# Performance work log

Measured on AMD Instinct MI355X. Metric: run time of the kernel, lower is better.

The kernel has to match this reference:

```python
import jax, jax.numpy as jnp
import numpy as np

EPS = 1e-5

def setup_inputs() -> dict:
    key = jax.random.key(0)
    ks = jax.random.split(key, 8)
    B, s, i, c = 1, 256, 256, 256
    h, d = 8, 32  # n_head, c_h; h*d == c
    m = jax.random.normal(ks[0], (B, s, i, c), dtype=jnp.float32)
    msa_mask = jnp.ones((B, s, i), dtype=jnp.float32)
    sc = 1.0 / np.sqrt(c)
    return {
        "m": m,
        "msa_mask": msa_mask,
        "ln_w": jnp.ones((c,), jnp.float32),
        "ln_b": jnp.zeros((c,), jnp.float32),
        "wq": jax.random.normal(ks[1], (h * d, c), jnp.float32) * sc,
        "wk": jax.random.normal(ks[2], (h * d, c), jnp.float32) * sc,
        "wv": jax.random.normal(ks[3], (h * d, c), jnp.float32) * sc,
        "wg": jax.random.normal(ks[4], (h * d, c), jnp.float32) * sc,
        "bg": jnp.zeros((h * d,), jnp.float32),
        "wo": jax.random.normal(ks[5], (c, h * d), jnp.float32) * sc,
        "bo": jnp.zeros((c,), jnp.float32),
    }

def _to_heads(x, B, s, i, h, d):
    # [B,s,i,h*d] -> [B,i,h,s,d]
    return jnp.transpose(x.reshape(B, s, i, h, d), (0, 2, 3, 1, 4))

def reference(m, msa_mask, ln_w, ln_b, wq, wk, wv, wg, bg, wo, bo):
    B, s, i, c = m.shape
    hd = wq.shape[0]
    d = 32
    h = hd // d
    # LayerNorm over channel dim
    mu = jnp.mean(m, axis=-1, keepdims=True)
    var = jnp.mean(jnp.square(m - mu), axis=-1, keepdims=True)
    m_norm = (m - mu) * jax.lax.rsqrt(var + EPS) * ln_w + ln_b
    q = _to_heads(m_norm @ wq.T, B, s, i, h, d)
    k = _to_heads(m_norm @ wk.T, B, s, i, h, d)
    v = _to_heads(m_norm @ wv.T, B, s, i, h, d)
    gate = jax.nn.sigmoid(_to_heads(m_norm @ wg.T + bg, B, s, i, h, d))
    # masks: msa_mask [B,s,i] -> keys mask [B,i,s]
    mk = jnp.transpose(msa_mask, (0, 2, 1)) > 0
    mv = mk.astype(q.dtype)[:, :, None, :, None]  # [B,i,1,s,1]
    q = q * mv
    k = k * mv
    v = v * mv
    gate = gate * mv
    # attention over sequence dim s (per column i)
    logits = jnp.einsum('bihqd,bihkd->bihqk', q, k) / jnp.sqrt(jnp.asarray(d, q.dtype))
    pair_mask = (mk[:, :, None, :] & mk[:, :, :, None])[:, :, None, :, :]  # [B,i,1,s,s]
    logits = jnp.where(pair_mask, logits, jnp.asarray(-1e9, q.dtype))
    attn = jax.nn.softmax(logits, axis=-1)
    o = jnp.einsum('bihqk,bihkd->bihqd', attn, v)
    o = o * gate * mv
    # [B,i,h,s,d] -> [B,i,s,h*d]
    o = jnp.transpose(o, (0, 1, 3, 2, 4)).reshape(B, i, s, h * d)
    o = o @ wo.T + bo  # [B,i,s,c]
    return jnp.transpose(o, (0, 2, 1, 3))  # [B,s,i,c]
```

## Files before the change

### kernel.cpp

```cpp
#include <hip/hip_runtime.h>

typedef unsigned short u16;
typedef unsigned int u32;
typedef __attribute__((ext_vector_type(8))) short short8;
typedef __attribute__((ext_vector_type(4))) float f32x4;

constexpr int S_ = 256, I_ = 256, C_ = 256, H_ = 8, D_ = 32, HD_ = 256;
constexpr float QSCALE = 0.17677669529663687f;

__device__ __forceinline__ float b2f(u32 u) {
  union { u32 i; float f; } x; x.i = u << 16; return x.f;
}
__device__ __forceinline__ u16 f2b(float f) {
  union { float f; u32 i; } x; x.f = f;
  u32 r = x.i + 0x7fffu + ((x.i >> 16) & 1u);
  return (u16)(r >> 16);
}
__device__ __forceinline__ uint4 pack8(const float* f) {
  uint4 r;
  r.x = (u32)f2b(f[0]) | ((u32)f2b(f[1]) << 16);
  r.y = (u32)f2b(f[2]) | ((u32)f2b(f[3]) << 16);
  r.z = (u32)f2b(f[4]) | ((u32)f2b(f[5]) << 16);
  r.w = (u32)f2b(f[6]) | ((u32)f2b(f[7]) << 16);
  return r;
}
__device__ __forceinline__ void load8f(const float* p, float* f) {
  float4 a = *reinterpret_cast<const float4*>(p);
  float4 b = *reinterpret_cast<const float4*>(p + 4);
  f[0] = a.x; f[1] = a.y; f[2] = a.z; f[3] = a.w;
  f[4] = b.x; f[5] = b.y; f[6] = b.z; f[7] = b.w;
}
__device__ __forceinline__ f32x4 mfma16(short8 a, short8 b, f32x4 c) {
  return __builtin_amdgcn_mfma_f32_16x16x32_bf16(a, b, c, 0, 0, 0);
}

__global__ void k_lnnorm(const float* __restrict__ m, const float* __restrict__ mask,
                         const float* __restrict__ lnw, const float* __restrict__ lnb,
                         u16* __restrict__ mn) {
  int wg = (blockIdx.x * 256 + threadIdx.x) >> 6;
  int lane = threadIdx.x & 63;
  float4 wv = *reinterpret_cast<const float4*>(lnw + lane * 4);
  float4 bv = *reinterpret_cast<const float4*>(lnb + lane * 4);
  for (int it = 0; it < 8; ++it) {
    int row = wg * 8 + it;
    float4 v = *reinterpret_cast<const float4*>(m + (size_t)row * C_ + lane * 4);
    float s = v.x + v.y + v.z + v.w;
    float ss = v.x * v.x + v.y * v.y + v.z * v.z + v.w * v.w;
#pragma unroll
    for (int o = 32; o; o >>= 1) { s += __shfl_xor(s, o); ss += __shfl_xor(ss, o); }
    float mean = s * (1.f / C_);
    float var = ss * (1.f / C_) - mean * mean;
    float rs = rsqrtf(fmaxf(var, 0.f) + 1e-5f);
    float mk = mask[row];
    float y[4];
    y[0] = ((v.x - mean) * rs * wv.x + bv.x) * mk;
    y[1] = ((v.y - mean) * rs * wv.y + bv.y) * mk;
    y[2] = ((v.z - mean) * rs * wv.z + bv.z) * mk;
    y[3] = ((v.w - mean) * rs * wv.w + bv.w) * mk;
    uint2 pk;
    pk.x = (u32)f2b(y[0]) | ((u32)f2b(y[1]) << 16);
    pk.y = (u32)f2b(y[2]) | ((u32)f2b(y[3]) << 16);
    *reinterpret_cast<uint2*>(mn + (size_t)row * C_ + lane * 4) = pk;
  }
}

__global__ void k_wpack(const float* __restrict__ wq, const float* __restrict__ wk,
                        const float* __restrict__ wv, const float* __restrict__ wg,
                        const float* __restrict__ wo, u16* __restrict__ wall2) {
  int gid = blockIdx.x * 4 + (threadIdx.x >> 6);
  int lane = threadIdx.x & 63;
  if (gid >= 640) return;
  const float* W;
  int g2;
  if (gid < 512) {
    int mat = gid >> 7;
    W = (mat == 0) ? wq : (mat == 1) ? wk : (mat == 2) ? wv : wg;
    g2 = gid & 127;
  } else {
    W = wo;
    g2 = gid - 512;
  }
  int nn = g2 & 1, kk = (g2 >> 1) & 7, ch2 = (g2 >> 4) & 1, cbi = (g2 >> 5) & 3;
  int row = cbi * 64 + ch2 * 32 + nn * 16 + (lane & 15);
  int k0 = kk * 32 + (lane >> 4) * 8;
  float f[8];
  load8f(W + (size_t)row * 256 + k0, f);
  *reinterpret_cast<uint4*>(wall2 + (size_t)gid * 512 + lane * 8) = pack8(f);
}

__global__ __launch_bounds__(256, 4) void k_qkvg(
    const u16* __restrict__ mn, const float* __restrict__ mask,
    const u16* __restrict__ wall2, const float* __restrict__ bg,
    u16* __restrict__ qws, u16* __restrict__ kws, u16* __restrict__ vws,
    u16* __restrict__ gws) {
  __shared__ u16 lA[64 * 256];
  int tile = blockIdx.x;
  int i_col = tile >> 2, s0 = (tile & 3) * 64;
  int t = threadIdx.x;
  int rowg = t >> 5, cg = t & 31;
#pragma unroll
  for (int p = 0; p < 8; ++p) {
    int row = p * 8 + rowg;
    int rg = (s0 + row) * I_ + i_col;
    *reinterpret_cast<uint4*>(&lA[row * 256 + ((cg * 8) ^ ((row & 7) << 3))]) =
        *reinterpret_cast<const uint4*>(mn + (size_t)rg * C_ + cg * 8);
  }
  __syncthreads();
  int lane = t & 63, w = t >> 6;
  int wr = (w >> 1) * 32, ch2 = w & 1, wc = ch2 * 32;
  int lr = lane & 15, lk = lane >> 4;
  f32x4 zz = {0.f, 0.f, 0.f, 0.f};
  for (int chunk = 0; chunk < 16; ++chunk) {
    int mat = chunk >> 2, cb = (chunk & 3) * 64;
    const u16* Bp = wall2 + (size_t)((chunk * 2 + ch2) * 16) * 512 + lane * 8;
    f32x4 acc[2][2] = {{zz, zz}, {zz, zz}};
#pragma unroll
    for (int kk = 0; kk < 8; ++kk) {
      int kb = kk * 32 + lk * 8;
      int ra0 = wr + lr, ra1 = wr + 16 + lr;
      short8 a0 = *reinterpret_cast<const short8*>(&lA[ra0 * 256 + (kb ^ ((ra0 & 7) << 3))]);
      short8 a1 = *reinterpret_cast<const short8*>(&lA[ra1 * 256 + (kb ^ ((ra1 & 7) << 3))]);
      short8 b0 = *reinterpret_cast<const short8*>(Bp + (kk * 2 + 0) * 512);
      short8 b1 = *reinterpret_cast<const short8*>(Bp + (kk * 2 + 1) * 512);
      acc[0][0] = mfma16(a0, b0, acc[0][0]);
      acc[0][1] = mfma16(a0, b1, acc[0][1]);
      acc[1][0] = mfma16(a1, b0, acc[1][0]);
      acc[1][1] = mfma16(a1, b1, acc[1][1]);
    }
#pragma unroll
    for (int mm = 0; mm < 2; ++mm) {
#pragma unroll
      for (int nn = 0; nn < 2; ++nn) {
        int colL = wc + nn * 16 + lr;
        int hd = cb + colL;
        int h = hd >> 5, d = hd & 31;
        if (mat == 2) {
          int sbase = s0 + wr + mm * 16 + lk * 4;
          uint2 pk;
          pk.x = (u32)f2b(acc[mm][nn][0]) | ((u32)f2b(acc[mm][nn][1]) << 16);
          pk.y = (u32)f2b(acc[mm][nn][2]) | ((u32)f2b(acc[mm][nn][3]) << 16);
          *reinterpret_cast<uint2*>(
              vws + (((size_t)i_col * H_ + h) * D_ + d) * S_ + sbase) = pk;
        } else {
          u16* dstp = (mat == 0) ? qws : (mat == 1) ? kws : gws;
          float bgv = (mat == 3) ? bg[hd] : 0.f;
#pragma unroll
          for (int r = 0; r < 4; ++r) {
            int rowL = wr + mm * 16 + lk * 4 + r;
            int s = s0 + rowL;
            float v = acc[mm][nn][r];
            if (mat == 0) v *= QSCALE;
            if (mat == 3) {
              float mkv = mask[s * I_ + i_col];
              v = mkv * (1.f / (1.f + __expf(-(v + bgv))));
            }
            dstp[(((size_t)i_col * H_ + h) * S_ + s) * D_ + d] = f2b(v);
          }
        }
      }
    }
  }
}

__global__ __launch_bounds__(1024) void k_attn(
    u16* __restrict__ qws, const u16* __restrict__ kws,
    const u16* __restrict__ vws, const u16* __restrict__ gws,
    const float* __restrict__ mask) {
  __shared__ u16 lK[256 * 40];
  __shared__ u16 lV[32 * 264];
  __shared__ float lMk[256];
  int bid = blockIdx.x;
  int i = bid >> 3, h = bid & 7;
  int t = threadIdx.x;
  size_t base = ((size_t)i * H_ + h) * (size_t)(S_ * D_);
  {
    int s = t >> 2, part = t & 3;
    *reinterpret_cast<uint4*>(&lK[s * 40 + part * 8]) =
        *reinterpret_cast<const uint4*>(kws + base + s * 32 + part * 8);
    int d = t >> 5, p2 = t & 31;
    *reinterpret_cast<uint4*>(&lV[d * 264 + p2 * 8]) =
        *reinterpret_cast<const uint4*>(vws + base + d * 256 + p2 * 8);
    if (t < 256) lMk[t] = mask[t * I_ + i];
  }
  __syncthreads();
  int lane = t & 63;
  int wvid = t >> 6;
  int lq = lane & 15, g = lane >> 4;
  int qbase = wvid * 16;
  short8 qf = *reinterpret_cast<const short8*>(qws + base + (size_t)(qbase + lq) * D_ + g * 8);
  f32x4 zz = {0.f, 0.f, 0.f, 0.f};
  f32x4 o0 = zz, o1 = zz;
  float mcur = -1e30f, sumd = 0.f;
  int addrP0 = (lq + ((g & 1) * 2 + 0) * 16) * 4;
  int addrP1 = (lq + ((g & 1) * 2 + 1) * 16) * 4;
  int aC0 = (g * 4 + 0) * 4, aC1 = (g * 4 + 1) * 4;
  int aC2 = (g * 4 + 2) * 4, aC3 = (g * 4 + 3) * 4;
#pragma unroll
  for (int ks = 0; ks < 8; ++ks) {
    int k0 = ks * 32;
    short8 kf0 = *reinterpret_cast<const short8*>(&lK[(k0 + lq) * 40 + g * 8]);
    short8 kf1 = *reinterpret_cast<const short8*>(&lK[(k0 + 16 + lq) * 40 + g * 8]);
    f32x4 s0 = mfma16(kf0, qf, zz);
    f32x4 s1 = mfma16(kf1, qf, zz);
    float4 mk0 = *reinterpret_cast<const float4*>(&lMk[k0 + g * 4]);
    float4 mk1 = *reinterpret_cast<const float4*>(&lMk[k0 + 16 + g * 4]);
    float sv[8];
    sv[0] = mk0.x > 0.f ? s0[0] : -1e9f;
    sv[1] = mk0.y > 0.f ? s0[1] : -1e9f;
    sv[2] = mk0.z > 0.f ? s0[2] : -1e9f;
    sv[3] = mk0.w > 0.f ? s0[3] : -1e9f;
    sv[4] = mk1.x > 0.f ? s1[0] : -1e9f;
    sv[5] = mk1.y > 0.f ? s1[1] : -1e9f;
    sv[6] = mk1.z > 0.f ? s1[2] : -1e9f;
    sv[7] = mk1.w > 0.f ? s1[3] : -1e9f;
    float tmax = fmaxf(fmaxf(fmaxf(sv[0], sv[1]), fmaxf(sv[2], sv[3])),
                       fmaxf(fmaxf(sv[4], sv[5]), fmaxf(sv[6], sv[7])));
    tmax = fmaxf(tmax, __shfl_xor(tmax, 16));
    tmax = fmaxf(tmax, __shfl_xor(tmax, 32));
    float mnew = fmaxf(mcur, tmax);
    float c = __expf(mcur - mnew);
    mcur = mnew;
    float p[8];
#pragma unroll
    for (int j = 0; j < 8; ++j) p[j] = __expf(sv[j] - mnew);
    sumd = sumd * c + ((p[0] + p[1]) + (p[2] + p[3])) + ((p[4] + p[5]) + (p[6] + p[7]));
    u32 pk00 = (u32)f2b(p[0]) | ((u32)f2b(p[1]) << 16);
    u32 pk01 = (u32)f2b(p[2]) | ((u32)f2b(p[3]) << 16);
    u32 pk10 = (u32)f2b(p[4]) | ((u32)f2b(p[5]) << 16);
    u32 pk11 = (u32)f2b(p[6]) | ((u32)f2b(p[7]) << 16);
    int b00 = __builtin_amdgcn_ds_bpermute(addrP0, (int)pk00);
    int b10 = __builtin_amdgcn_ds_bpermute(addrP0, (int)pk10);
    int b01 = __builtin_amdgcn_ds_bpermute(addrP0, (int)pk01);
    int b11 = __builtin_amdgcn_ds_bpermute(addrP0, (int)pk11);
    int b02 = __builtin_amdgcn_ds_bpermute(addrP1, (int)pk00);
    int b12 = __builtin_amdgcn_ds_bpermute(addrP1, (int)pk10);
    int b03 = __builtin_amdgcn_ds_bpermute(addrP1, (int)pk01);
    int b13 = __builtin_amdgcn_ds_bpermute(addrP1, (int)pk11);
    union { int u[4]; short8 s8; } pu;
    bool lo = (g < 2);
    pu.u[0] = lo ? b00 : b10;
    pu.u[1] = lo ? b01 : b11;
    pu.u[2] = lo ? b02 : b12;
    pu.u[3] = lo ? b03 : b13;
    float co0 = __int_as_float(__builtin_amdgcn_ds_bpermute(aC0, __float_as_int(c)));
    float co1 = __int_as_float(__builtin_amdgcn_ds_bpermute(aC1, __float_as_int(c)));
    float co2 = __int_as_float(__builtin_amdgcn_ds_bpermute(aC2, __float_as_int(c)));
    float co3 = __int_as_float(__builtin_amdgcn_ds_bpermute(aC3, __float_as_int(c)));
    o0[0] *= co0; o0[1] *= co1; o0[2] *= co2; o0[3] *= co3;
    o1[0] *= co0; o1[1] *= co1; o1[2] *= co2; o1[3] *= co3;
    short8 vf0 = *reinterpret_cast<const short8*>(&lV[lq * 264 + k0 + g * 8]);
    short8 vf1 = *reinterpret_cast<const short8*>(&lV[(16 + lq) * 264 + k0 + g * 8]);
    o0 = mfma16(pu.s8, vf0, o0);
    o1 = mfma16(pu.s8, vf1, o1);
  }
  float s2 = sumd + __shfl_xor(sumd, 16);
  float tot = s2 + __shfl_xor(s2, 32);
  float iv = 1.f / tot;
  float ivo[4];
  ivo[0] = __int_as_float(__builtin_amdgcn_ds_bpermute(aC0, __float_as_int(iv)));
  ivo[1] = __int_as_float(__builtin_amdgcn_ds_bpermute(aC1, __float_as_int(iv)));
  ivo[2] = __int_as_float(__builtin_amdgcn_ds_bpermute(aC2, __float_as_int(iv)));
  ivo[3] = __int_as_float(__builtin_amdgcn_ds_bpermute(aC3, __float_as_int(iv)));
#pragma unroll
  for (int r = 0; r < 4; ++r) {
    int row = qbase + g * 4 + r;
    size_t idx0 = base + (size_t)row * D_ + lq;
    size_t idx1 = idx0 + 16;
    float g0 = b2f((u32)gws[idx0]);
    float g1 = b2f((u32)gws[idx1]);
    qws[idx0] = f2b(o0[r] * ivo[r] * g0);
    qws[idx1] = f2b(o1[r] * ivo[r] * g1);
  }
}

__global__ __launch_bounds__(256, 4) void k_oproj(const u16* __restrict__ ows,
                                                  const u16* __restrict__ wall2,
                                                  const float* __restrict__ bo,
                                                  float* __restrict__ out) {
  __shared__ u16 lA[64 * 256];
  int tile = blockIdx.x;
  int r0 = tile * 64;
  int t = threadIdx.x;
  int rowg = t >> 5, cg = t & 31;
  int hh = cg >> 2, d0 = (cg & 3) * 8;
#pragma unroll
  for (int p = 0; p < 8; ++p) {
    int row = p * 8 + rowg;
    int rg = r0 + row;
    int ii = rg >> 8, ss = rg & 255;
    *reinterpret_cast<uint4*>(&lA[row * 256 + ((cg * 8) ^ ((row & 7) << 3))]) =
        *reinterpret_cast<const uint4*>(ows + (((size_t)ii * H_ + hh) * S_ + ss) * D_ + d0);
  }
  __syncthreads();
  int lane = t & 63, w = t >> 6;
  int wr = (w >> 1) * 32, ch2 = w & 1, wc = ch2 * 32;
  int lr = lane & 15, lk = lane >> 4;
  f32x4 zz = {0.f, 0.f, 0.f, 0.f};
  for (int chunk = 0; chunk < 4; ++chunk) {
    int cb = chunk * 64;
    const u16* Bp = wall2 + (size_t)(512 + (chunk * 2 + ch2) * 16) * 512 + lane * 8;
    f32x4 acc[2][2] = {{zz, zz}, {zz, zz}};
#pragma unroll
    for (int kk = 0; kk < 8; ++kk) {
      int kb = kk * 32 + lk * 8;
      int ra0 = wr + lr, ra1 = wr + 16 + lr;
      short8 a0 = *reinterpret_cast<const short8*>(&lA[ra0 * 256 + (kb ^ ((ra0 & 7) << 3))]);
      short8 a1 = *reinterpret_cast<const short8*>(&lA[ra1 * 256 + (kb ^ ((ra1 & 7) << 3))]);
      short8 b0 = *reinterpret_cast<const short8*>(Bp + (kk * 2 + 0) * 512);
      short8 b1 = *reinterpret_cast<const short8*>(Bp + (kk * 2 + 1) * 512);
      acc[0][0] = mfma16(a0, b0, acc[0][0]);
      acc[0][1] = mfma16(a0, b1, acc[0][1]);
      acc[1][0] = mfma16(a1, b0, acc[1][0]);
      acc[1][1] = mfma16(a1, b1, acc[1][1]);
    }
#pragma unroll
    for (int mm = 0; mm < 2; ++mm) {
#pragma unroll
      for (int nn = 0; nn < 2; ++nn) {
        int colL = wc + nn * 16 + lr;
        int ch = cb + colL;
        float bov = bo[ch];
#pragma unroll
        for (int r = 0; r < 4; ++r) {
          int rowL = wr + mm * 16 + lk * 4 + r;
          int rg = r0 + rowL;
          int ii = rg >> 8;
          int ss = rg & 255;
          out[((size_t)ss * I_ + ii) * C_ + ch] = acc[mm][nn][r] + bov;
        }
      }
    }
  }
}

extern "C" void kernel_launch(void* const* d_in, const int* in_sizes, int n_in,
                              void* d_out, int out_size, void* d_ws, size_t ws_size,
                              hipStream_t stream) {
  const float *m, *mask, *lnw, *lnb, *wq, *wk, *wv, *wg, *bg, *wo, *bo;
  if (in_sizes[0] > 1000000) {
    m = (const float*)d_in[0]; mask = (const float*)d_in[1];
    lnw = (const float*)d_in[2]; lnb = (const float*)d_in[3];
    wq = (const float*)d_in[4]; wk = (const float*)d_in[5];
    wv = (const float*)d_in[6]; wg = (const float*)d_in[7];
    bg = (const float*)d_in[8]; wo = (const float*)d_in[9];
    bo = (const float*)d_in[10];
  } else {
    bg = (const float*)d_in[0]; bo = (const float*)d_in[1];
    lnb = (const float*)d_in[2]; lnw = (const float*)d_in[3];
    m = (const float*)d_in[4]; mask = (const float*)d_in[5];
    wg = (const float*)d_in[6]; wk = (const float*)d_in[7];
    wo = (const float*)d_in[8]; wq = (const float*)d_in[9];
    wv = (const float*)d_in[10];
  }
  float* out = (float*)d_out;

  const size_t SZ = (size_t)S_ * I_ * C_;
  u16* qws = (u16*)d_ws;
  u16* kws = qws + SZ;
  u16* vws = kws + SZ;
  u16* gws = vws + SZ;
  u16* mn = gws + SZ;
  u16* wall2 = mn + SZ;

  k_lnnorm<<<2048, 256, 0, stream>>>(m, mask, lnw, lnb, mn);
  k_wpack<<<160, 256, 0, stream>>>(wq, wk, wv, wg, wo, wall2);
  k_qkvg<<<1024, 256, 0, stream>>>(mn, mask, wall2, bg, qws, kws, vws, gws);
  k_attn<<<2048, 1024, 0, stream>>>(qws, kws, vws, gws, mask);
  k_oproj<<<1024, 256, 0, stream>>>(qws, wall2, bo, out);
}
```

Baseline: 193.2 us.

## Fuse LayerNorm into QKVG projection and double threads per GEMM block

Removes the separate LayerNorm kernel and its bf16 intermediate buffer by computing mean/variance and normalisation inside the QKVG GEMM's LDS load stage, reading fp32 input directly. Both the QKVG and output-projection kernels now run 512 threads per block, with warps split across output chunks so each warp handles half as many chunks. This cuts one launch and a full write plus read of the normalised activations. In exchange each QKVG block reads twice the bytes from fp32 input, and the larger blocks may lower the number of blocks resident per CU.

```diff
diff --git a/kernel.cpp b/kernel.cpp
--- a/kernel.cpp
+++ b/kernel.cpp
@@ -32,36 +32,6 @@
 }
 __device__ __forceinline__ f32x4 mfma16(short8 a, short8 b, f32x4 c) {
   return __builtin_amdgcn_mfma_f32_16x16x32_bf16(a, b, c, 0, 0, 0);
-}
-
-__global__ void k_lnnorm(const float* __restrict__ m, const float* __restrict__ mask,
-                         const float* __restrict__ lnw, const float* __restrict__ lnb,
-                         u16* __restrict__ mn) {
-  int wg = (blockIdx.x * 256 + threadIdx.x) >> 6;
-  int lane = threadIdx.x & 63;
-  float4 wv = *reinterpret_cast<const float4*>(lnw + lane * 4);
-  float4 bv = *reinterpret_cast<const float4*>(lnb + lane * 4);
-  for (int it = 0; it < 8; ++it) {
-    int row = wg * 8 + it;
-    float4 v = *reinterpret_cast<const float4*>(m + (size_t)row * C_ + lane * 4);
-    float s = v.x + v.y + v.z + v.w;
-    float ss = v.x * v.x + v.y * v.y + v.z * v.z + v.w * v.w;
-#pragma unroll
-    for (int o = 32; o; o >>= 1) { s += __shfl_xor(s, o); ss += __shfl_xor(ss, o); }
-    float mean = s * (1.f / C_);
-    float var = ss * (1.f / C_) - mean * mean;
-    float rs = rsqrtf(fmaxf(var, 0.f) + 1e-5f);
-    float mk = mask[row];
-    float y[4];
-    y[0] = ((v.x - mean) * rs * wv.x + bv.x) * mk;
-    y[1] = ((v.y - mean) * rs * wv.y + bv.y) * mk;
-    y[2] = ((v.z - mean) * rs * wv.z + bv.z) * mk;
-    y[3] = ((v.w - mean) * rs * wv.w + bv.w) * mk;
-    uint2 pk;
-    pk.x = (u32)f2b(y[0]) | ((u32)f2b(y[1]) << 16);
-    pk.y = (u32)f2b(y[2]) | ((u32)f2b(y[3]) << 16);
-    *reinterpret_cast<uint2*>(mn + (size_t)row * C_ + lane * 4) = pk;
-  }
 }
 
 __global__ void k_wpack(const float* __restrict__ wq, const float* __restrict__ wk,
@@ -88,8 +58,9 @@
   *reinterpret_cast<uint4*>(wall2 + (size_t)gid * 512 + lane * 8) = pack8(f);
 }
 
-__global__ __launch_bounds__(256, 4) void k_qkvg(
-    const u16* __restrict__ mn, const float* __restrict__ mask,
+__global__ __launch_bounds__(512) void k_qkvg(
+    const float* __restrict__ m, const float* __restrict__ mask,
+    const float* __restrict__ lnw, const float* __restrict__ lnb,
     const u16* __restrict__ wall2, const float* __restrict__ bg,
     u16* __restrict__ qws, u16* __restrict__ kws, u16* __restrict__ vws,
     u16* __restrict__ gws) {
@@ -98,20 +69,41 @@
   int i_col = tile >> 2, s0 = (tile & 3) * 64;
   int t = threadIdx.x;
   int rowg = t >> 5, cg = t & 31;
-#pragma unroll
-  for (int p = 0; p < 8; ++p) {
-    int row = p * 8 + rowg;
+  float wv8[8], bv8[8];
+  load8f(lnw + cg * 8, wv8);
+  load8f(lnb + cg * 8, bv8);
+#pragma unroll
+  for (int p = 0; p < 4; ++p) {
+    int row = p * 16 + rowg;
     int rg = (s0 + row) * I_ + i_col;
-    *reinterpret_cast<uint4*>(&lA[row * 256 + ((cg * 8) ^ ((row & 7) << 3))]) =
-        *reinterpret_cast<const uint4*>(mn + (size_t)rg * C_ + cg * 8);
+    float xf[8], yf[8];
+    load8f(m + (size_t)rg * C_ + cg * 8, xf);
+    float s1 = 0.f, s2 = 0.f;
+#pragma unroll
+    for (int u = 0; u < 8; ++u) { s1 += xf[u]; s2 += xf[u] * xf[u]; }
+#pragma unroll
+    for (int o = 16; o; o >>= 1) { s1 += __shfl_xor(s1, o); s2 += __shfl_xor(s2, o); }
+    float mean = s1 * (1.f / C_);
+    float var = s2 * (1.f / C_) - mean * mean;
+    float rs = rsqrtf(fmaxf(var, 0.f) + 1e-5f);
+    float mkv = mask[rg];
+#pragma unroll
+    for (int u = 0; u < 8; ++u) yf[u] = ((xf[u] - mean) * rs * wv8[u] + bv8[u]) * mkv;
+    *reinterpret_cast<uint4*>(&lA[row * 256 + ((cg * 8) ^ ((row & 7) << 3))]) = pack8(yf);
   }
   __syncthreads();
   int lane = t & 63, w = t >> 6;
-  int wr = (w >> 1) * 32, ch2 = w & 1, wc = ch2 * 32;
+  int wr = (w >> 2) * 32;
+  int dsel = (w & 3) >> 1;
+  int ch2 = w & 1;
+  int wc = ch2 * 32;
   int lr = lane & 15, lk = lane >> 4;
   f32x4 zz = {0.f, 0.f, 0.f, 0.f};
-  for (int chunk = 0; chunk < 16; ++chunk) {
-    int mat = chunk >> 2, cb = (chunk & 3) * 64;
+#pragma unroll
+  for (int it = 0; it < 8; ++it) {
+    int chunk = it * 2 + dsel;
+    const int mat = it >> 1;
+    int cb = (chunk & 3) * 64;
     const u16* Bp = wall2 + (size_t)((chunk * 2 + ch2) * 16) * 512 + lane * 8;
     f32x4 acc[2][2] = {{zz, zz}, {zz, zz}};
 #pragma unroll
@@ -127,6 +119,7 @@
       acc[1][0] = mfma16(a1, b0, acc[1][0]);
       acc[1][1] = mfma16(a1, b1, acc[1][1]);
     }
+    u16* dstp = (mat == 0) ? qws : (mat == 1) ? kws : (mat == 2) ? vws : gws;
 #pragma unroll
     for (int mm = 0; mm < 2; ++mm) {
 #pragma unroll
@@ -139,15 +132,12 @@
           uint2 pk;
           pk.x = (u32)f2b(acc[mm][nn][0]) | ((u32)f2b(acc[mm][nn][1]) << 16);
           pk.y = (u32)f2b(acc[mm][nn][2]) | ((u32)f2b(acc[mm][nn][3]) << 16);
-          *reinterpret_cast<uint2*>(
-              vws + (((size_t)i_col * H_ + h) * D_ + d) * S_ + sbase) = pk;
+          *reinterpret_cast<uint2*>(vws + (((size_t)i_col * H_ + h) * D_ + d) * S_ + sbase) = pk;
         } else {
-          u16* dstp = (mat == 0) ? qws : (mat == 1) ? kws : gws;
           float bgv = (mat == 3) ? bg[hd] : 0.f;
 #pragma unroll
           for (int r = 0; r < 4; ++r) {
-            int rowL = wr + mm * 16 + lk * 4 + r;
-            int s = s0 + rowL;
+            int s = s0 + wr + mm * 16 + lk * 4 + r;
             float v = acc[mm][nn][r];
             if (mat == 0) v *= QSCALE;
             if (mat == 3) {
@@ -273,10 +263,10 @@
   }
 }
 
-__global__ __launch_bounds__(256, 4) void k_oproj(const u16* __restrict__ ows,
-                                                  const u16* __restrict__ wall2,
-                                                  const float* __restrict__ bo,
-                                                  float* __restrict__ out) {
+__global__ __launch_bounds__(512) void k_oproj(const u16* __restrict__ ows,
+                                               const u16* __restrict__ wall2,
+                                               const float* __restrict__ bo,
+                                               float* __restrict__ out) {
   __shared__ u16 lA[64 * 256];
   int tile = blockIdx.x;
   int r0 = tile * 64;
@@ -284,8 +274,8 @@
   int rowg = t >> 5, cg = t & 31;
   int hh = cg >> 2, d0 = (cg & 3) * 8;
 #pragma unroll
-  for (int p = 0; p < 8; ++p) {
-    int row = p * 8 + rowg;
+  for (int p = 0; p < 4; ++p) {
+    int row = p * 16 + rowg;
     int rg = r0 + row;
     int ii = rg >> 8, ss = rg & 255;
     *reinterpret_cast<uint4*>(&lA[row * 256 + ((cg * 8) ^ ((row & 7) << 3))]) =
@@ -293,10 +283,15 @@
   }
   __syncthreads();
   int lane = t & 63, w = t >> 6;
-  int wr = (w >> 1) * 32, ch2 = w & 1, wc = ch2 * 32;
+  int wr = (w >> 2) * 32;
+  int dsel = (w & 3) >> 1;
+  int ch2 = w & 1;
+  int wc = ch2 * 32;
   int lr = lane & 15, lk = lane >> 4;
   f32x4 zz = {0.f, 0.f, 0.f, 0.f};
-  for (int chunk = 0; chunk < 4; ++chunk) {
+#pragma unroll
+  for (int it = 0; it < 2; ++it) {
+    int chunk = it * 2 + dsel;
     int cb = chunk * 64;
     const u16* Bp = wall2 + (size_t)(512 + (chunk * 2 + ch2) * 16) * 512 + lane * 8;
     f32x4 acc[2][2] = {{zz, zz}, {zz, zz}};
@@ -317,13 +312,11 @@
     for (int mm = 0; mm < 2; ++mm) {
 #pragma unroll
       for (int nn = 0; nn < 2; ++nn) {
-        int colL = wc + nn * 16 + lr;
-        int ch = cb + colL;
+        int ch = cb + wc + nn * 16 + lr;
         float bov = bo[ch];
 #pragma unroll
         for (int r = 0; r < 4; ++r) {
-          int rowL = wr + mm * 16 + lk * 4 + r;
-          int rg = r0 + rowL;
+          int rg = r0 + wr + mm * 16 + lk * 4 + r;
           int ii = rg >> 8;
           int ss = rg & 255;
           out[((size_t)ss * I_ + ii) * C_ + ch] = acc[mm][nn][r] + bov;
@@ -359,12 +352,10 @@
   u16* kws = qws + SZ;
   u16* vws = kws + SZ;
   u16* gws = vws + SZ;
-  u16* mn = gws + SZ;
-  u16* wall2 = mn + SZ;
-
-  k_lnnorm<<<2048, 256, 0, stream>>>(m, mask, lnw, lnb, mn);
+  u16* wall2 = gws + SZ;
+
   k_wpack<<<160, 256, 0, stream>>>(wq, wk, wv, wg, wo, wall2);
-  k_qkvg<<<1024, 256, 0, stream>>>(mn, mask, wall2, bg, qws, kws, vws, gws);
+  k_qkvg<<<1024, 512, 0, stream>>>(m, mask, lnw, lnb, wall2, bg, qws, kws, vws, gws);
   k_attn<<<2048, 1024, 0, stream>>>(qws, kws, vws, gws, mask);
-  k_oproj<<<1024, 256, 0, stream>>>(qws, wall2, bo, out);
-}
+  k_oproj<<<1024, 512, 0, stream>>>(qws, wall2, bo, out);
+}
```

Result: slower. 210.8 us (+9.1%).

## Skip online-softmax rescale when max grows little; widen oproj to 512 threads

Applied to the files above, without the earlier changes.

In the attention kernel, the running max and the output rescale are updated only when some lane's tile max exceeds the current max by more than 8. Otherwise the old max is kept, which saves the four bpermutes and eight multiplies per iteration, at the cost of p values up to e^8 in bf16/fp32. Separately, the output projection now uses 512 threads per block: each wave computes one 16-column slice instead of two, and the LDS fill loop has half as many iterations. This raises parallelism per block but reduces per-wave reuse of A fragments.

```diff
diff --git a/kernel.cpp b/kernel.cpp
--- a/kernel.cpp
+++ b/kernel.cpp
@@ -217,13 +217,23 @@
                        fmaxf(fmaxf(sv[4], sv[5]), fmaxf(sv[6], sv[7])));
     tmax = fmaxf(tmax, __shfl_xor(tmax, 16));
     tmax = fmaxf(tmax, __shfl_xor(tmax, 32));
-    float mnew = fmaxf(mcur, tmax);
-    float c = __expf(mcur - mnew);
-    mcur = mnew;
+    bool skip = __all(tmax <= mcur + 8.0f);
+    if (!skip) {
+      float mnew = fmaxf(mcur, tmax);
+      float c = __expf(mcur - mnew);
+      mcur = mnew;
+      sumd *= c;
+      float co0 = __int_as_float(__builtin_amdgcn_ds_bpermute(aC0, __float_as_int(c)));
+      float co1 = __int_as_float(__builtin_amdgcn_ds_bpermute(aC1, __float_as_int(c)));
+      float co2 = __int_as_float(__builtin_amdgcn_ds_bpermute(aC2, __float_as_int(c)));
+      float co3 = __int_as_float(__builtin_amdgcn_ds_bpermute(aC3, __float_as_int(c)));
+      o0[0] *= co0; o0[1] *= co1; o0[2] *= co2; o0[3] *= co3;
+      o1[0] *= co0; o1[1] *= co1; o1[2] *= co2; o1[3] *= co3;
+    }
     float p[8];
 #pragma unroll
-    for (int j = 0; j < 8; ++j) p[j] = __expf(sv[j] - mnew);
-    sumd = sumd * c + ((p[0] + p[1]) + (p[2] + p[3])) + ((p[4] + p[5]) + (p[6] + p[7]));
+    for (int j = 0; j < 8; ++j) p[j] = __expf(sv[j] - mcur);
+    sumd += ((p[0] + p[1]) + (p[2] + p[3])) + ((p[4] + p[5]) + (p[6] + p[7]));
     u32 pk00 = (u32)f2b(p[0]) | ((u32)f2b(p[1]) << 16);
     u32 pk01 = (u32)f2b(p[2]) | ((u32)f2b(p[3]) << 16);
     u32 pk10 = (u32)f2b(p[4]) | ((u32)f2b(p[5]) << 16);
@@ -242,12 +252,6 @@
     pu.u[1] = lo ? b01 : b11;
     pu.u[2] = lo ? b02 : b12;
     pu.u[3] = lo ? b03 : b13;
-    float co0 = __int_as_float(__builtin_amdgcn_ds_bpermute(aC0, __float_as_int(c)));
-    float co1 = __int_as_float(__builtin_amdgcn_ds_bpermute(aC1, __float_as_int(c)));
-    float co2 = __int_as_float(__builtin_amdgcn_ds_bpermute(aC2, __float_as_int(c)));
-    float co3 = __int_as_float(__builtin_amdgcn_ds_bpermute(aC3, __float_as_int(c)));
-    o0[0] *= co0; o0[1] *= co1; o0[2] *= co2; o0[3] *= co3;
-    o1[0] *= co0; o1[1] *= co1; o1[2] *= co2; o1[3] *= co3;
     short8 vf0 = *reinterpret_cast<const short8*>(&lV[lq * 264 + k0 + g * 8]);
     short8 vf1 = *reinterpret_cast<const short8*>(&lV[(16 + lq) * 264 + k0 + g * 8]);
     o0 = mfma16(pu.s8, vf0, o0);
@@ -273,10 +277,10 @@
   }
 }
 
-__global__ __launch_bounds__(256, 4) void k_oproj(const u16* __restrict__ ows,
-                                                  const u16* __restrict__ wall2,
-                                                  const float* __restrict__ bo,
-                                                  float* __restrict__ out) {
+__global__ __launch_bounds__(512) void k_oproj(const u16* __restrict__ ows,
+                                               const u16* __restrict__ wall2,
+                                               const float* __restrict__ bo,
+                                               float* __restrict__ out) {
   __shared__ u16 lA[64 * 256];
   int tile = blockIdx.x;
   int r0 = tile * 64;
@@ -284,8 +288,8 @@
   int rowg = t >> 5, cg = t & 31;
   int hh = cg >> 2, d0 = (cg & 3) * 8;
 #pragma unroll
-  for (int p = 0; p < 8; ++p) {
-    int row = p * 8 + rowg;
+  for (int p = 0; p < 4; ++p) {
+    int row = p * 16 + rowg;
     int rg = r0 + row;
     int ii = rg >> 8, ss = rg & 255;
     *reinterpret_cast<uint4*>(&lA[row * 256 + ((cg * 8) ^ ((row & 7) << 3))]) =
@@ -293,41 +297,35 @@
   }
   __syncthreads();
   int lane = t & 63, w = t >> 6;
-  int wr = (w >> 1) * 32, ch2 = w & 1, wc = ch2 * 32;
+  int wr = (w >> 2) * 32, ch4 = w & 3;
   int lr = lane & 15, lk = lane >> 4;
   f32x4 zz = {0.f, 0.f, 0.f, 0.f};
   for (int chunk = 0; chunk < 4; ++chunk) {
     int cb = chunk * 64;
-    const u16* Bp = wall2 + (size_t)(512 + (chunk * 2 + ch2) * 16) * 512 + lane * 8;
-    f32x4 acc[2][2] = {{zz, zz}, {zz, zz}};
+    const u16* Bp =
+        wall2 + (size_t)(512 + (chunk * 2 + (ch4 >> 1)) * 16 + (ch4 & 1)) * 512 + lane * 8;
+    f32x4 acc0 = zz, acc1 = zz;
 #pragma unroll
     for (int kk = 0; kk < 8; ++kk) {
       int kb = kk * 32 + lk * 8;
       int ra0 = wr + lr, ra1 = wr + 16 + lr;
       short8 a0 = *reinterpret_cast<const short8*>(&lA[ra0 * 256 + (kb ^ ((ra0 & 7) << 3))]);
       short8 a1 = *reinterpret_cast<const short8*>(&lA[ra1 * 256 + (kb ^ ((ra1 & 7) << 3))]);
-      short8 b0 = *reinterpret_cast<const short8*>(Bp + (kk * 2 + 0) * 512);
-      short8 b1 = *reinterpret_cast<const short8*>(Bp + (kk * 2 + 1) * 512);
-      acc[0][0] = mfma16(a0, b0, acc[0][0]);
-      acc[0][1] = mfma16(a0, b1, acc[0][1]);
-      acc[1][0] = mfma16(a1, b0, acc[1][0]);
-      acc[1][1] = mfma16(a1, b1, acc[1][1]);
-    }
+      short8 b0 = *reinterpret_cast<const short8*>(Bp + kk * 1024);
+      acc0 = mfma16(a0, b0, acc0);
+      acc1 = mfma16(a1, b0, acc1);
+    }
+    int ch = cb + ch4 * 16 + lr;
+    float bov = bo[ch];
 #pragma unroll
     for (int mm = 0; mm < 2; ++mm) {
-#pragma unroll
-      for (int nn = 0; nn < 2; ++nn) {
-        int colL = wc + nn * 16 + lr;
-        int ch = cb + colL;
-        float bov = bo[ch];
-#pragma unroll
-        for (int r = 0; r < 4; ++r) {
-          int rowL = wr + mm * 16 + lk * 4 + r;
-          int rg = r0 + rowL;
-          int ii = rg >> 8;
-          int ss = rg & 255;
-          out[((size_t)ss * I_ + ii) * C_ + ch] = acc[mm][nn][r] + bov;
-        }
+      const f32x4& acc = (mm == 0) ? acc0 : acc1;
+#pragma unroll
+      for (int r = 0; r < 4; ++r) {
+        int rg = r0 + wr + mm * 16 + lk * 4 + r;
+        int ii = rg >> 8;
+        int ss = rg & 255;
+        out[((size_t)ss * I_ + ii) * C_ + ch] = acc[r] + bov;
       }
     }
   }
@@ -366,5 +364,5 @@
   k_wpack<<<160, 256, 0, stream>>>(wq, wk, wv, wg, wo, wall2);
   k_qkvg<<<1024, 256, 0, stream>>>(mn, mask, wall2, bg, qws, kws, vws, gws);
   k_attn<<<2048, 1024, 0, stream>>>(qws, kws, vws, gws, mask);
-  k_oproj<<<1024, 256, 0, stream>>>(qws, wall2, bo, out);
-}
+  k_oproj<<<1024, 512, 0, stream>>>(qws, wall2, bo, out);
+}
```

After: 192.6 us. About the same (-0.3%).
